# Performance work log

Hardware: AMD Instinct MI355X
Metric: run time of the kernel (lower is better)

Reference implementation:

```python
import jax, jax.numpy as jnp
from jax import lax
import numpy as np

OUT_CH = 16      # texture_features
INTER = 32       # texture_features_intermediate
TEXDIM = 1024    # texture_dimensions
IN_SIZE = 76


def _leaky(x):
    return jnp.where(x >= 0, x, 0.02 * x)


def grid_sample_bilinear_border(tex, grid):
    """torch.nn.functional.grid_sample, mode='bilinear', padding_mode='border',
    align_corners=False.  tex: (N,C,H,W); grid: (N,Ho,Wo,2) with (x,y) in [-1,1].
    N == 1 here; vectorized over H,W via fancy indexing."""
    N, C, H, W = tex.shape
    x, y = grid[..., 0], grid[..., 1]
    # unnormalize (align_corners=False)
    ix = ((x + 1.0) * W - 1.0) * 0.5
    iy = ((y + 1.0) * H - 1.0) * 0.5
    # border padding: clamp continuous coords
    ix = jnp.clip(ix, 0.0, W - 1.0)
    iy = jnp.clip(iy, 0.0, H - 1.0)
    x0 = jnp.floor(ix); y0 = jnp.floor(iy)
    wx = ix - x0; wy = iy - y0
    x0i = jnp.clip(x0, 0, W - 1).astype(jnp.int32)
    x1i = jnp.clip(x0 + 1, 0, W - 1).astype(jnp.int32)
    y0i = jnp.clip(y0, 0, H - 1).astype(jnp.int32)
    y1i = jnp.clip(y0 + 1, 0, H - 1).astype(jnp.int32)
    t = tex[0]  # (C,H,W)
    v00 = t[:, y0i[0], x0i[0]]  # (C,Ho,Wo)
    v01 = t[:, y0i[0], x1i[0]]
    v10 = t[:, y1i[0], x0i[0]]
    v11 = t[:, y1i[0], x1i[0]]
    wx = wx[0][None]; wy = wy[0][None]  # (1,Ho,Wo) broadcast over C
    out = (v00 * (1 - wx) * (1 - wy) + v01 * wx * (1 - wy)
           + v10 * (1 - wx) * wy + v11 * wx * wy)
    return out[None]  # (1,C,Ho,Wo)


def setup_inputs() -> dict:
    key = jax.random.key(0)
    ks = jax.random.split(key, 11)
    expressions = jax.random.normal(ks[0], (1, IN_SIZE), jnp.float32)
    audio_features = jax.random.normal(ks[1], (1, 16), jnp.float32)
    uv_inputs = jax.random.uniform(ks[2], (1, 2, 1024, 1024), jnp.float32, -1.0, 1.0)
    data = jax.random.normal(ks[3], (1, INTER, TEXDIM, TEXDIM), jnp.float32)
    def lin(kw, kb, fo, fi):
        s = 1.0 / np.sqrt(fi).astype(np.float32)
        return (jax.random.uniform(kw, (fo, fi), jnp.float32, -s, s),
                jax.random.uniform(kb, (fo,), jnp.float32, -s, s))
    W1, b1 = lin(ks[4], ks[5], 128, IN_SIZE)
    W2, b2 = lin(ks[6], ks[7], 64, 128)
    W3, b3 = lin(ks[8], ks[9], OUT_CH * 4 * 4 * INTER, 64)
    return {"expressions": expressions, "audio_features": audio_features,
            "uv_inputs": uv_inputs, "data": data,
            "W1": W1, "b1": b1, "W2": W2, "b2": b2, "W3": W3, "b3": b3}


def reference(expressions, audio_features, uv_inputs, data, W1, b1, W2, b2, W3, b3):
    # tiny MLP -> dynamic 4x4 conv filter
    h = expressions.reshape(1, 1, -1)
    h = _leaky(h @ W1.T + b1)
    h = _leaky(h @ W2.T + b2)
    f = jnp.tanh(h @ W3.T + b3)
    conv_filter = f.reshape(OUT_CH, INTER, 4, 4)
    # conv2d(data, filter, stride=1, padding=2) -> (1, OUT_CH, D+1, D+1)
    tex_eval = lax.conv_general_dilated(
        data, conv_filter, window_strides=(1, 1), padding=((2, 2), (2, 2)),
        dimension_numbers=("NCHW", "OIHW", "NCHW"))
    # grid: stack x (chan 0) and y (chan 1) along last dim
    grid = jnp.stack([uv_inputs[:, 0], uv_inputs[:, 1]], axis=3)  # (1,Ho,Wo,2)
    return grid_sample_bilinear_border(tex_eval, grid)
```

## Files before the change

kernel.cpp:

```cpp
#include <hip/hip_runtime.h>
#include <math.h>

#define NPX   1048576
#define TD    1025
#define PW    35
#define PH    19
#define DPAD  1028
#define ROWB  65792
#define DP_OFF 33673216

typedef _Float16 half8 __attribute__((ext_vector_type(8)));
typedef float    f32x4 __attribute__((ext_vector_type(4)));

__device__ __forceinline__ void load_lds16(const void* g, void* lds) {
    __builtin_amdgcn_global_load_lds(
        (const __attribute__((address_space(1))) void*)g,
        (__attribute__((address_space(3))) void*)lds, 16, 0, 0);
}

__global__ __launch_bounds__(256) void mlp_kernel(
    const float* __restrict__ expr,
    const float* __restrict__ W1, const float* __restrict__ b1,
    const float* __restrict__ W2, const float* __restrict__ b2,
    const float* __restrict__ W3, const float* __restrict__ b3,
    float* __restrict__ filt_t)
{
    __shared__ float sx[76];
    __shared__ float sh1[128];
    __shared__ float sh2[64];
    int t = threadIdx.x;
    if (t < 76) sx[t] = expr[t];
    __syncthreads();
    if (t < 128) {
        float a = b1[t];
        const float* w = W1 + t * 76;
        #pragma unroll 4
        for (int i = 0; i < 76; ++i) a += sx[i] * w[i];
        sh1[t] = a >= 0.f ? a : 0.02f * a;
    }
    __syncthreads();
    if (t < 64) {
        float a = b2[t];
        const float* w = W2 + t * 128;
        #pragma unroll 4
        for (int i = 0; i < 128; ++i) a += sh1[i] * w[i];
        sh2[t] = a >= 0.f ? a : 0.02f * a;
    }
    __syncthreads();
    int o = blockIdx.x * 256 + t;
    float a = b3[o];
    const float* w = W3 + o * 64;
    #pragma unroll 4
    for (int i = 0; i < 64; ++i) a += sh2[i] * w[i];
    a = tanhf(a);
    int oc = o >> 9;
    int k  = o & 511;
    filt_t[k * 16 + oc] = a;
}

__global__ __launch_bounds__(256) void ffrag_kernel(
    const float* __restrict__ filt_t, _Float16* __restrict__ ffrag_g)
{
    int idx = blockIdx.x * 256 + threadIdx.x;
    int kk = idx >> 6;
    int l  = idx & 63;
    int q  = l >> 4, oc = l & 15;
    half8 h;
    #pragma unroll
    for (int j = 0; j < 8; ++j) {
        int ic = q * 8 + j;
        h[j] = (_Float16)filt_t[(ic * 16 + kk) * 16 + oc];
    }
    *(half8*)&ffrag_g[idx * 8] = h;
}

__global__ __launch_bounds__(256) void repack_kernel(
    const float* __restrict__ data, _Float16* __restrict__ Dp)
{
    __shared__ _Float16 s[256 * 32];
    int tid = threadIdx.x;
    int Y = blockIdx.y;
    int X = blockIdx.x * 256 + tid;
    int y = Y - 2, x = X - 2;
    bool ok = ((unsigned)y < 1024u) && ((unsigned)x < 1024u);
    const float* dp = data + ((size_t)y << 10) + x;

    float v[32];
    #pragma unroll
    for (int j = 0; j < 32; ++j) v[j] = 0.f;
    if (ok) {
        #pragma unroll
        for (int j = 0; j < 32; ++j) v[j] = dp[(size_t)j * NPX];
    }
    #pragma unroll
    for (int g = 0; g < 4; ++g) {
        half8 h;
        #pragma unroll
        for (int j = 0; j < 8; ++j) h[j] = (_Float16)v[g * 8 + j];
        int chunk = tid * 4 + g;
        int sw = chunk ^ ((chunk >> 3) & 7);
        *(half8*)((char*)s + sw * 16) = h;
    }
    __syncthreads();
    char* rowbase = (char*)Dp + (size_t)Y * ROWB + blockIdx.x * 16384;
    int lim = ROWB - blockIdx.x * 16384;
    #pragma unroll
    for (int i = 0; i < 4; ++i) {
        int off = tid * 16 + i * 4096;
        if (off < lim) {
            int chunk = tid + i * 256;
            int sw = chunk ^ ((chunk >> 3) & 7);
            *(uint4*)(rowbase + off) = *(uint4*)((char*)s + sw * 16);
        }
    }
}

__global__ __launch_bounds__(256, 3) void conv_mfma_kernel(
    const _Float16* __restrict__ Dp,
    const _Float16* __restrict__ ffrag_g,
    _Float16* __restrict__ tex)
{
    __shared__ _Float16 sp[PH * PW * 32];

    int tid = threadIdx.x;
    int l = tid & 63, w = tid >> 6;
    int ox0 = blockIdx.x * 32;
    int oy0 = blockIdx.y * 16;

    half8 bfrag[16];
    #pragma unroll
    for (int kk = 0; kk < 16; ++kk)
        bfrag[kk] = *(const half8*)&ffrag_g[kk * 512 + l * 8];

    for (int r = w; r < PH; r += 4) {
        int gy = min(oy0 + r, DPAD - 1);
        const char* grow = (const char*)Dp + (size_t)gy * ROWB;
        _Float16* lrow = sp + r * (PW * 32);
        #pragma unroll
        for (int c = 0; c < 3; ++c) {
            int off = ox0 * 64 + c * 1024 + l * 16;
            off = min(off, ROWB - 16);
            if (c < 2 || l < 12)
                load_lds16(grow + off, (char*)lrow + c * 1024);
        }
    }
    __syncthreads();

    int lane15 = l & 15;
    int q = l >> 4;

    f32x4 acc[8];
    #pragma unroll
    for (int t = 0; t < 8; ++t) acc[t] = (f32x4){0.f, 0.f, 0.f, 0.f};

    #pragma unroll 4
    for (int kk = 0; kk < 16; ++kk) {
        int ky = kk >> 2, kx = kk & 3;
        #pragma unroll
        for (int t = 0; t < 8; ++t) {
            int pc = (w * 4 + (t >> 1) + ky) * PW + (t & 1) * 16 + lane15 + kx;
            half8 af = *(half8*)&sp[pc * 32 + q * 8];
            acc[t] = __builtin_amdgcn_mfma_f32_16x16x32_f16(af, bfrag[kk], acc[t], 0, 0, 0);
        }
    }

    #pragma unroll
    for (int t = 0; t < 8; ++t) {
        int oy = oy0 + w * 4 + (t >> 1);
        if (oy > 1024) continue;
        int pxb = ox0 + (t & 1) * 16 + q * 4;
        #pragma unroll
        for (int r = 0; r < 4; ++r) {
            int px = pxb + r;
            if (px > 1024) continue;
            tex[((size_t)oy * TD + px) * 16 + lane15] = (_Float16)acc[t][r];
        }
    }
}

__global__ __launch_bounds__(256) void sample_kernel(
    const float* __restrict__ uv,
    const _Float16* __restrict__ tex,
    float* __restrict__ out)
{
    int p0 = blockIdx.x * 512 + threadIdx.x;
    half8 v[2][8];
    float W[2][4];
    #pragma unroll
    for (int i = 0; i < 2; ++i) {
        int p = p0 + i * 256;
        float x = uv[p], y = uv[NPX + p];
        float ix = fminf(fmaxf(((x + 1.f) * 1025.f - 1.f) * 0.5f, 0.f), 1024.f);
        float iy = fminf(fmaxf(((y + 1.f) * 1025.f - 1.f) * 0.5f, 0.f), 1024.f);
        float fx0 = floorf(ix), fy0 = floorf(iy);
        float wx = ix - fx0, wy = iy - fy0;
        int x0 = (int)fx0, y0 = (int)fy0;
        int x1 = min(x0 + 1, 1024), y1 = min(y0 + 1, 1024);
        const half8* t00 = (const half8*)(tex + ((size_t)y0 * TD + x0) * 16);
        const half8* t01 = (const half8*)(tex + ((size_t)y0 * TD + x1) * 16);
        const half8* t10 = (const half8*)(tex + ((size_t)y1 * TD + x0) * 16);
        const half8* t11 = (const half8*)(tex + ((size_t)y1 * TD + x1) * 16);
        v[i][0] = t00[0]; v[i][1] = t00[1];
        v[i][2] = t01[0]; v[i][3] = t01[1];
        v[i][4] = t10[0]; v[i][5] = t10[1];
        v[i][6] = t11[0]; v[i][7] = t11[1];
        W[i][0] = (1.f - wx) * (1.f - wy);
        W[i][1] = wx * (1.f - wy);
        W[i][2] = (1.f - wx) * wy;
        W[i][3] = wx * wy;
    }
    #pragma unroll
    for (int i = 0; i < 2; ++i) {
        int p = p0 + i * 256;
        #pragma unroll
        for (int h = 0; h < 2; ++h) {
            #pragma unroll
            for (int c = 0; c < 8; ++c) {
                float r = (float)v[i][0 + h][c] * W[i][0]
                        + (float)v[i][2 + h][c] * W[i][1]
                        + (float)v[i][4 + h][c] * W[i][2]
                        + (float)v[i][6 + h][c] * W[i][3];
                out[(size_t)(h * 8 + c) * NPX + p] = r;
            }
        }
    }
}

extern "C" void kernel_launch(void* const* d_in, const int* in_sizes, int n_in,
                              void* d_out, int out_size, void* d_ws, size_t ws_size,
                              hipStream_t stream) {
    const float* expr = (const float*)d_in[0];
    const float* uv   = (const float*)d_in[2];
    const float* data = (const float*)d_in[3];
    const float* W1   = (const float*)d_in[4];
    const float* b1   = (const float*)d_in[5];
    const float* W2   = (const float*)d_in[6];
    const float* b2   = (const float*)d_in[7];
    const float* W3   = (const float*)d_in[8];
    const float* b3   = (const float*)d_in[9];
    float* out = (float*)d_out;

    float* filt_t      = (float*)d_ws;
    _Float16* ffrag_g  = (_Float16*)((char*)d_ws + 32768);
    _Float16* tex      = (_Float16*)((char*)d_ws + 49152);
    _Float16* Dp       = (_Float16*)((char*)d_ws + DP_OFF);

    mlp_kernel<<<32, 256, 0, stream>>>(expr, W1, b1, W2, b2, W3, b3, filt_t);
    ffrag_kernel<<<4, 256, 0, stream>>>(filt_t, ffrag_g);
    repack_kernel<<<dim3(5, DPAD), 256, 0, stream>>>(data, Dp);
    conv_mfma_kernel<<<dim3(33, 65), 256, 0, stream>>>(Dp, ffrag_g, tex);
    sample_kernel<<<NPX / 512, 256, 0, stream>>>(uv, tex, out);
}
```

Measured before the change: 389.7 us.

## Fuse filter fragment packing into MLP, add nontemporal loads/stores, simplify sampler

The MLP kernel now writes the fp16 MFMA filter fragments directly, which removes the separate ffrag kernel launch and the fp32 intermediate buffer. The repack and sample kernels use nontemporal loads and stores for data that is streamed once, to reduce cache pollution. The sampler now handles one pixel per thread with a larger launch count and an occupancy hint in place of two pixels per thread. The trade-off is less memory-level parallelism per thread in exchange for more resident waves.

After: 362.4 us. 7.0% less time.

```diff
diff --git a/kernel.cpp b/kernel.cpp
--- a/kernel.cpp
+++ b/kernel.cpp
@@ -23,7 +23,7 @@
     const float* __restrict__ W1, const float* __restrict__ b1,
     const float* __restrict__ W2, const float* __restrict__ b2,
     const float* __restrict__ W3, const float* __restrict__ b3,
-    float* __restrict__ filt_t)
+    _Float16* __restrict__ ffrag_g)
 {
     __shared__ float sx[76];
     __shared__ float sh1[128];
@@ -54,24 +54,9 @@
     for (int i = 0; i < 64; ++i) a += sh2[i] * w[i];
     a = tanhf(a);
     int oc = o >> 9;
-    int k  = o & 511;
-    filt_t[k * 16 + oc] = a;
-}
-
-__global__ __launch_bounds__(256) void ffrag_kernel(
-    const float* __restrict__ filt_t, _Float16* __restrict__ ffrag_g)
-{
-    int idx = blockIdx.x * 256 + threadIdx.x;
-    int kk = idx >> 6;
-    int l  = idx & 63;
-    int q  = l >> 4, oc = l & 15;
-    half8 h;
-    #pragma unroll
-    for (int j = 0; j < 8; ++j) {
-        int ic = q * 8 + j;
-        h[j] = (_Float16)filt_t[(ic * 16 + kk) * 16 + oc];
-    }
-    *(half8*)&ffrag_g[idx * 8] = h;
+    int ic = (o >> 4) & 31;
+    int kk = o & 15;
+    ffrag_g[(size_t)(kk * 64 + (ic >> 3) * 16 + oc) * 8 + (ic & 7)] = (_Float16)a;
 }
 
 __global__ __launch_bounds__(256) void repack_kernel(
@@ -90,7 +75,7 @@
     for (int j = 0; j < 32; ++j) v[j] = 0.f;
     if (ok) {
         #pragma unroll
-        for (int j = 0; j < 32; ++j) v[j] = dp[(size_t)j * NPX];
+        for (int j = 0; j < 32; ++j) v[j] = __builtin_nontemporal_load(&dp[(size_t)j * NPX]);
     }
     #pragma unroll
     for (int g = 0; g < 4; ++g) {
@@ -178,51 +163,44 @@
     }
 }
 
-__global__ __launch_bounds__(256) void sample_kernel(
+__global__ __launch_bounds__(256, 6) void sample_kernel(
     const float* __restrict__ uv,
     const _Float16* __restrict__ tex,
     float* __restrict__ out)
 {
-    int p0 = blockIdx.x * 512 + threadIdx.x;
-    half8 v[2][8];
-    float W[2][4];
-    #pragma unroll
-    for (int i = 0; i < 2; ++i) {
-        int p = p0 + i * 256;
-        float x = uv[p], y = uv[NPX + p];
-        float ix = fminf(fmaxf(((x + 1.f) * 1025.f - 1.f) * 0.5f, 0.f), 1024.f);
-        float iy = fminf(fmaxf(((y + 1.f) * 1025.f - 1.f) * 0.5f, 0.f), 1024.f);
-        float fx0 = floorf(ix), fy0 = floorf(iy);
-        float wx = ix - fx0, wy = iy - fy0;
-        int x0 = (int)fx0, y0 = (int)fy0;
-        int x1 = min(x0 + 1, 1024), y1 = min(y0 + 1, 1024);
-        const half8* t00 = (const half8*)(tex + ((size_t)y0 * TD + x0) * 16);
-        const half8* t01 = (const half8*)(tex + ((size_t)y0 * TD + x1) * 16);
-        const half8* t10 = (const half8*)(tex + ((size_t)y1 * TD + x0) * 16);
-        const half8* t11 = (const half8*)(tex + ((size_t)y1 * TD + x1) * 16);
-        v[i][0] = t00[0]; v[i][1] = t00[1];
-        v[i][2] = t01[0]; v[i][3] = t01[1];
-        v[i][4] = t10[0]; v[i][5] = t10[1];
-        v[i][6] = t11[0]; v[i][7] = t11[1];
-        W[i][0] = (1.f - wx) * (1.f - wy);
-        W[i][1] = wx * (1.f - wy);
-        W[i][2] = (1.f - wx) * wy;
-        W[i][3] = wx * wy;
-    }
-    #pragma unroll
-    for (int i = 0; i < 2; ++i) {
-        int p = p0 + i * 256;
-        #pragma unroll
-        for (int h = 0; h < 2; ++h) {
-            #pragma unroll
-            for (int c = 0; c < 8; ++c) {
-                float r = (float)v[i][0 + h][c] * W[i][0]
-                        + (float)v[i][2 + h][c] * W[i][1]
-                        + (float)v[i][4 + h][c] * W[i][2]
-                        + (float)v[i][6 + h][c] * W[i][3];
-                out[(size_t)(h * 8 + c) * NPX + p] = r;
-            }
-        }
+    int p = blockIdx.x * 256 + threadIdx.x;
+    float x = __builtin_nontemporal_load(&uv[p]);
+    float y = __builtin_nontemporal_load(&uv[NPX + p]);
+    float ix = fminf(fmaxf(((x + 1.f) * 1025.f - 1.f) * 0.5f, 0.f), 1024.f);
+    float iy = fminf(fmaxf(((y + 1.f) * 1025.f - 1.f) * 0.5f, 0.f), 1024.f);
+    float fx0 = floorf(ix), fy0 = floorf(iy);
+    float wx = ix - fx0, wy = iy - fy0;
+    int x0 = (int)fx0, y0 = (int)fy0;
+    int x1 = min(x0 + 1, 1024), y1 = min(y0 + 1, 1024);
+
+    const half8* t00 = (const half8*)(tex + ((size_t)y0 * TD + x0) * 16);
+    const half8* t01 = (const half8*)(tex + ((size_t)y0 * TD + x1) * 16);
+    const half8* t10 = (const half8*)(tex + ((size_t)y1 * TD + x0) * 16);
+    const half8* t11 = (const half8*)(tex + ((size_t)y1 * TD + x1) * 16);
+
+    half8 v0 = t00[0], v1 = t00[1];
+    half8 v2 = t01[0], v3 = t01[1];
+    half8 v4 = t10[0], v5 = t10[1];
+    half8 v6 = t11[0], v7 = t11[1];
+
+    float w00 = (1.f - wx) * (1.f - wy);
+    float w01 = wx * (1.f - wy);
+    float w10 = (1.f - wx) * wy;
+    float w11 = wx * wy;
+
+    #pragma unroll
+    for (int c = 0; c < 8; ++c) {
+        float r0 = (float)v0[c] * w00 + (float)v2[c] * w01
+                 + (float)v4[c] * w10 + (float)v6[c] * w11;
+        float r1 = (float)v1[c] * w00 + (float)v3[c] * w01
+                 + (float)v5[c] * w10 + (float)v7[c] * w11;
+        __builtin_nontemporal_store(r0, &out[(size_t)c * NPX + p]);
+        __builtin_nontemporal_store(r1, &out[(size_t)(c + 8) * NPX + p]);
     }
 }
 
@@ -240,14 +218,12 @@
     const float* b3   = (const float*)d_in[9];
     float* out = (float*)d_out;
 
-    float* filt_t      = (float*)d_ws;
-    _Float16* ffrag_g  = (_Float16*)((char*)d_ws + 32768);
+    _Float16* ffrag_g  = (_Float16*)d_ws;
     _Float16* tex      = (_Float16*)((char*)d_ws + 49152);
     _Float16* Dp       = (_Float16*)((char*)d_ws + DP_OFF);
 
-    mlp_kernel<<<32, 256, 0, stream>>>(expr, W1, b1, W2, b2, W3, b3, filt_t);
-    ffrag_kernel<<<4, 256, 0, stream>>>(filt_t, ffrag_g);
+    mlp_kernel<<<32, 256, 0, stream>>>(expr, W1, b1, W2, b2, W3, b3, ffrag_g);
     repack_kernel<<<dim3(5, DPAD), 256, 0, stream>>>(data, Dp);
     conv_mfma_kernel<<<dim3(33, 65), 256, 0, stream>>>(Dp, ffrag_g, tex);
-    sample_kernel<<<NPX / 512, 256, 0, stream>>>(uv, tex, out);
-}
+    sample_kernel<<<NPX / 256, 256, 0, stream>>>(uv, tex, out);
+}
```
